# Kernel tuning notes

Measured on AMD Instinct MI355X. Metric: run time of the kernel, lower is better.

The kernel has to match this reference:

```python
import jax, jax.numpy as jnp
import numpy as np

N_NODES = 40000
N_EDGES = 1_600_000
F_DIM = 64          # num_features per node; MLP input is 2*F_DIM = 128
HIDDEN = 64
BETA = 1.0          # temperature tmp passed to concrete_sample


def setup_inputs() -> dict:
    key = jax.random.key(0)
    k_e, k_n, k_w1, k_w2 = jax.random.split(key, 4)
    # unique edge list (matches torch COO->dense semantics exactly: no duplicate coords)
    rng = np.random.default_rng(0)
    keys = np.unique(rng.integers(0, N_NODES * N_NODES, size=int(N_EDGES * 1.1), dtype=np.int64))
    assert keys.size >= N_EDGES
    keys = keys[:N_EDGES]
    col = jnp.asarray((keys // N_NODES).astype(np.int32))
    row = jnp.asarray((keys % N_NODES).astype(np.int32))
    embed = jax.random.normal(k_e, (N_NODES, F_DIM), jnp.float32)
    # torch.rand noise for the concrete/gumbel-sigmoid sample (kept strictly inside (0,1))
    noise = jax.random.uniform(k_n, (N_EDGES,), jnp.float32, 1e-6, 1.0 - 1e-6)
    lim1 = 1.0 / np.sqrt(2 * F_DIM)
    W1 = jax.random.uniform(k_w1, (2 * F_DIM, HIDDEN), jnp.float32, -lim1, lim1)
    b1 = jnp.zeros((HIDDEN,), jnp.float32)
    lim2 = 1.0 / np.sqrt(HIDDEN)
    W2 = jax.random.uniform(k_w2, (HIDDEN, 1), jnp.float32, -lim2, lim2)
    b2 = jnp.zeros((1,), jnp.float32)
    return {"embed": embed, "W1": W1, "b1": b1, "W2": W2, "b2": b2,
            "noise": noise, "col": col, "row": row}


def reference(embed, W1, b1, W2, b2, noise, col, row):
    # --- gather + concat + 2-layer MLP (elayers) ---
    f12 = jnp.concatenate([embed[col], embed[row]], axis=-1)   # [E, 2F]
    h = jax.nn.relu(f12 @ W1 + b1)                              # [E, 64]
    log_alpha = (h @ W2 + b2).reshape(-1)                       # [E]
    # --- concrete_sample, training=True, sample_bias=0 ---
    gate = jnp.log(noise) - jnp.log1p(-noise)
    values = jax.nn.sigmoid((gate + log_alpha) / BETA)          # sparse_mask_values
    # --- symmetrization: sym = (M + M^T)/2 gathered back at (col,row) ---
    # Equivalent to torch's sparse->dense->transpose->gather, but done sparsely
    # via a reverse-edge lookup on sorted pair keys (edges are unique).
    n = embed.shape[0]
    keys = col * n + row                                        # int32-safe: n*n < 2^31
    order = jnp.argsort(keys)
    skeys = keys[order]
    svals = values[order]
    rkeys = row * n + col
    pos = jnp.clip(jnp.searchsorted(skeys, rkeys), 0, keys.shape[0] - 1)
    rev = jnp.where(skeys[pos] == rkeys, svals[pos], jnp.float32(0.0))
    edge_mask = (values + rev) * 0.5
    return edge_mask
```

## Files before the change

### kernel.cpp

```cpp
#include <hip/hip_runtime.h>
#include <hip/hip_bf16.h>


typedef __attribute__((ext_vector_type(2))) float f32x2;

#define EPAD 68

__global__ __launch_bounds__(256) void precompute_kernel(
        const float* __restrict__ embed,
        const float* __restrict__ W1,
        const float* __restrict__ b1,
        unsigned* __restrict__ Ptop,
        unsigned* __restrict__ Pbot,
        int n_nodes) {
    int t = threadIdx.x;

    __shared__ float W1s[128 * 64];
    __shared__ float E[64 * EPAD];
    int base = blockIdx.x * 64;

#pragma unroll
    for (int i = 0; i < 8; ++i) {
        int idx = i * 256 + t;
        ((float4*)W1s)[idx] = ((const float4*)W1)[idx];
    }
#pragma unroll
    for (int i = 0; i < 4; ++i) {
        int fi = i * 256 + t;
        int n = fi >> 4;
        int k4 = (fi & 15) * 4;
        float4 v;
        if (base + n < n_nodes)
            v = ((const float4*)(embed + (size_t)(base + n) * 64))[fi & 15];
        else
            v = make_float4(0.f, 0.f, 0.f, 0.f);
        *((float4*)(E + n * EPAD + k4)) = v;
    }
    __syncthreads();

    int tj = t & 15, tn = t >> 4;
    int j4 = tj * 4, n4 = tn * 4;
    float4 b1v = *(const float4*)(b1 + j4);
    float4 at[4], ab[4];
#pragma unroll
    for (int i = 0; i < 4; ++i) {
        at[i] = b1v;
        ab[i] = make_float4(0.f, 0.f, 0.f, 0.f);
    }

#pragma unroll 2
    for (int k4 = 0; k4 < 64; k4 += 4) {
        float4 e[4], wt[4], wb[4];
#pragma unroll
        for (int i = 0; i < 4; ++i) {
            e[i]  = *(const float4*)(E + (n4 + i) * EPAD + k4);
            wt[i] = *(const float4*)(W1s + (k4 + i) * 64 + j4);
            wb[i] = *(const float4*)(W1s + (64 + k4 + i) * 64 + j4);
        }
#pragma unroll
        for (int n = 0; n < 4; ++n) {
#pragma unroll
            for (int kk = 0; kk < 4; ++kk) {
                float ev = (kk == 0) ? e[n].x : (kk == 1) ? e[n].y
                         : (kk == 2) ? e[n].z : e[n].w;
                at[n].x += ev * wt[kk].x;  at[n].y += ev * wt[kk].y;
                at[n].z += ev * wt[kk].z;  at[n].w += ev * wt[kk].w;
                ab[n].x += ev * wb[kk].x;  ab[n].y += ev * wb[kk].y;
                ab[n].z += ev * wb[kk].z;  ab[n].w += ev * wb[kk].w;
            }
        }
    }

#pragma unroll
    for (int i = 0; i < 4; ++i) {
        int node = base + n4 + i;
        if (node >= n_nodes) break;
        int wt8 = __builtin_amdgcn_cvt_pk_fp8_f32(at[i].x, at[i].y, 0, false);
        wt8     = __builtin_amdgcn_cvt_pk_fp8_f32(at[i].z, at[i].w, wt8, true);
        Ptop[(size_t)node * 16 + tj] = (unsigned)wt8;
        int wb8 = __builtin_amdgcn_cvt_pk_fp8_f32(ab[i].x, ab[i].y, 0, false);
        wb8     = __builtin_amdgcn_cvt_pk_fp8_f32(ab[i].z, ab[i].w, wb8, true);
        Pbot[(size_t)node * 16 + tj] = (unsigned)wb8;
    }
}

#define DOTW(au, bu, wp, acc0, acc1) do {                             \
    f32x2 alo = __builtin_amdgcn_cvt_pk_f32_fp8((au), false);         \
    f32x2 ahi = __builtin_amdgcn_cvt_pk_f32_fp8((au), true);          \
    f32x2 blo = __builtin_amdgcn_cvt_pk_f32_fp8((bu), false);         \
    f32x2 bhi = __builtin_amdgcn_cvt_pk_f32_fp8((bu), true);          \
    f32x2 s0 = alo + blo, s1 = ahi + bhi;                             \
    s0 = __builtin_elementwise_max(s0, (f32x2)0.f);                   \
    s1 = __builtin_elementwise_max(s1, (f32x2)0.f);                   \
    acc0 += s0 * ((const f32x2*)(wp))[0];                             \
    acc1 += s1 * ((const f32x2*)(wp))[1];                             \
} while (0)

__global__ __launch_bounds__(256) void edge_value_kernel(
        const uint4* __restrict__ Ptop,
        const uint4* __restrict__ Pbot,
        const float* __restrict__ W2,
        const float* __restrict__ b2,
        const float* __restrict__ noise,
        const int* __restrict__ col,
        const int* __restrict__ row,
        unsigned short* __restrict__ row16,
        unsigned short* __restrict__ vals16,
        int* __restrict__ rowptr,
        int n_edges, int n_nodes, int rp_blocks) {
    int t = threadIdx.x;
    int bid = blockIdx.x;

    if (bid < rp_blocks) {
        int v = bid * 256 + t;
        if (v <= n_nodes) {
            int lo = 0, hi = n_edges;
            while (lo < hi) {
                int mid = (lo + hi) >> 1;
                if (col[mid] < v) lo = mid + 1; else hi = mid;
            }
            rowptr[v] = lo;
        }
        return;
    }

    int e = (bid - rp_blocks) * 256 + t;
    if (e >= n_edges) return;
    int c = col[e], r = row[e];
    const uint4* pt = Ptop + (size_t)c * 4;
    const uint4* pb = Pbot + (size_t)r * 4;
    f32x2 acc0 = {b2[0], 0.f}, acc1 = {0.f, 0.f};
    f32x2 acc2 = {0.f, 0.f},  acc3 = {0.f, 0.f};
#pragma unroll
    for (int g = 0; g < 4; ++g) {
        uint4 a = pt[g];
        uint4 b = pb[g];
        const float* w = W2 + g * 16;
        DOTW(a.x, b.x, w,      acc0, acc1);
        DOTW(a.y, b.y, w + 4,  acc2, acc3);
        DOTW(a.z, b.z, w + 8,  acc0, acc1);
        DOTW(a.w, b.w, w + 12, acc2, acc3);
    }
    f32x2 acc = (acc0 + acc1) + (acc2 + acc3);
    float la = acc.x + acc.y;
    float u = noise[e];
    float v = u / (u + (1.f - u) * __expf(-la));
    unsigned q = (unsigned)(v * 65535.f + 0.5f);
    if (q > 65535u) q = 65535u;
    row16[e]  = (unsigned short)r;
    vals16[e] = (unsigned short)q;
}

__device__ __forceinline__ float rev_scan(const unsigned short* __restrict__ row16,
                                          const unsigned short* __restrict__ vals16,
                                          int c, int lo, int hi, int g, int rv) {
    if (rv < c) {
        while (++g < hi) { rv = row16[g]; if (rv >= c) break; }
        return (g < hi && rv == c) ? (float)vals16[g] : 0.f;
    } else {
        while (rv > c && g > lo) rv = row16[--g];
        return (rv == c) ? (float)vals16[g] : 0.f;
    }
}

__global__ __launch_bounds__(256) void symmetrize_kernel(
        const int* __restrict__ col,
        const unsigned short* __restrict__ row16,
        const unsigned short* __restrict__ vals16,
        const int* __restrict__ rowptr,
        float* __restrict__ out,
        int n_edges, float inv_n) {
    int t = threadIdx.x;
    int e0 = blockIdx.x * 1024 + t;
    int c[4], r[4], lo[4], hi[4], g[4], pr[4];
    float vq[4];
    bool p[4], s[4];

#pragma unroll
    for (int i = 0; i < 4; ++i) {
        int e = e0 + i * 256;
        p[i] = e < n_edges;
        c[i] = 0; r[i] = 0; vq[i] = 0.f;
        if (p[i]) {
            c[i]  = col[e];
            r[i]  = row16[e];
            vq[i] = (float)vals16[e];
        }
    }
#pragma unroll
    for (int i = 0; i < 4; ++i) {
        lo[i] = 0; hi[i] = 0;
        if (p[i]) { lo[i] = rowptr[r[i]]; hi[i] = rowptr[r[i] + 1]; }
    }
#pragma unroll
    for (int i = 0; i < 4; ++i) {
        s[i] = p[i] && hi[i] > lo[i];
        g[i] = 0; pr[i] = 0;
        if (s[i]) {
            g[i] = lo[i] + (int)((float)c[i] * (float)(hi[i] - lo[i]) * inv_n);
            if (g[i] >= hi[i]) g[i] = hi[i] - 1;
            pr[i] = row16[g[i]];
        }
    }
#pragma unroll
    for (int i = 0; i < 4; ++i) {
        if (!p[i]) continue;
        float rev = s[i] ? rev_scan(row16, vals16, c[i], lo[i], hi[i], g[i], pr[i]) : 0.f;
        out[e0 + i * 256] = (vq[i] + rev) * (0.5f / 65535.f);
    }
}

extern "C" void kernel_launch(void* const* d_in, const int* in_sizes, int n_in,
                              void* d_out, int out_size, void* d_ws, size_t ws_size,
                              hipStream_t stream) {
    const float* embed = (const float*)d_in[0];
    const float* W1    = (const float*)d_in[1];
    const float* b1    = (const float*)d_in[2];
    const float* W2    = (const float*)d_in[3];
    const float* b2    = (const float*)d_in[4];
    const float* noise = (const float*)d_in[5];
    const int*   col   = (const int*)d_in[6];
    const int*   row   = (const int*)d_in[7];

    int n_nodes = in_sizes[0] / 64;
    int n_edges = in_sizes[5];
    float* out = (float*)d_out;

    char* ws = (char*)d_ws;
    size_t p_sz   = (size_t)n_nodes * 16 * sizeof(unsigned);
    size_t e16_sz = (size_t)n_edges * sizeof(unsigned short);
    unsigned*       Ptop   = (unsigned*)ws;
    unsigned*       Pbot   = (unsigned*)(ws + p_sz);
    unsigned short* row16  = (unsigned short*)(ws + 2 * p_sz);
    unsigned short* vals16 = (unsigned short*)(ws + 2 * p_sz + e16_sz);
    int*            rowptr = (int*)(ws + 2 * p_sz + 2 * e16_sz);

    int gemm_blocks = (n_nodes + 63) / 64;
    int rp_blocks   = (n_nodes + 256) / 256;

    precompute_kernel<<<gemm_blocks, 256, 0, stream>>>(
        embed, W1, b1, Ptop, Pbot, n_nodes);

    edge_value_kernel<<<rp_blocks + (n_edges + 255) / 256, 256, 0, stream>>>(
        (const uint4*)Ptop, (const uint4*)Pbot, W2, b2, noise, col, row,
        row16, vals16, rowptr, n_edges, n_nodes, rp_blocks);

    symmetrize_kernel<<<(n_edges + 1023) / 1024, 256, 0, stream>>>(
        col, row16, vals16, rowptr, out, n_edges, 1.0f / (float)n_nodes);
}
```

Measured before the change: 72.41 us.

## Write half-values in edge kernel and symmetrize only upper-triangle edges pairwise

The edge kernel now writes each edge's own half-value (or the full value on the diagonal) straight to the output. The symmetrize kernel handles only edges with col < row: it searches for the reverse edge and, on a match, adds each partner's contribution to both output slots. This roughly halves the reverse-edge searches and skips the output writes for unmatched edges. In exchange it uses read-modify-write updates to the output and scattered writes to the matched index, and its own value is now taken from the full-precision float rather than the 16-bit quantized copy.

```diff
diff --git a/kernel.cpp b/kernel.cpp
--- a/kernel.cpp
+++ b/kernel.cpp
@@ -106,6 +106,7 @@
         const int* __restrict__ row,
         unsigned short* __restrict__ row16,
         unsigned short* __restrict__ vals16,
+        float* __restrict__ out,
         int* __restrict__ rowptr,
         int n_edges, int n_nodes, int rp_blocks) {
     int t = threadIdx.x;
@@ -149,18 +150,7 @@
     if (q > 65535u) q = 65535u;
     row16[e]  = (unsigned short)r;
     vals16[e] = (unsigned short)q;
-}
-
-__device__ __forceinline__ float rev_scan(const unsigned short* __restrict__ row16,
-                                          const unsigned short* __restrict__ vals16,
-                                          int c, int lo, int hi, int g, int rv) {
-    if (rv < c) {
-        while (++g < hi) { rv = row16[g]; if (rv >= c) break; }
-        return (g < hi && rv == c) ? (float)vals16[g] : 0.f;
-    } else {
-        while (rv > c && g > lo) rv = row16[--g];
-        return (rv == c) ? (float)vals16[g] : 0.f;
-    }
+    out[e] = (c == r) ? v : 0.5f * v;
 }
 
 __global__ __launch_bounds__(256) void symmetrize_kernel(
@@ -173,28 +163,24 @@
     int t = threadIdx.x;
     int e0 = blockIdx.x * 1024 + t;
     int c[4], r[4], lo[4], hi[4], g[4], pr[4];
-    float vq[4];
-    bool p[4], s[4];
+    bool act[4], s[4];
 
 #pragma unroll
     for (int i = 0; i < 4; ++i) {
         int e = e0 + i * 256;
-        p[i] = e < n_edges;
-        c[i] = 0; r[i] = 0; vq[i] = 0.f;
-        if (p[i]) {
-            c[i]  = col[e];
-            r[i]  = row16[e];
-            vq[i] = (float)vals16[e];
-        }
+        bool p = e < n_edges;
+        c[i] = 0; r[i] = -1;
+        if (p) { c[i] = col[e]; r[i] = row16[e]; }
+        act[i] = p && c[i] < r[i];
     }
 #pragma unroll
     for (int i = 0; i < 4; ++i) {
         lo[i] = 0; hi[i] = 0;
-        if (p[i]) { lo[i] = rowptr[r[i]]; hi[i] = rowptr[r[i] + 1]; }
-    }
-#pragma unroll
-    for (int i = 0; i < 4; ++i) {
-        s[i] = p[i] && hi[i] > lo[i];
+        if (act[i]) { lo[i] = rowptr[r[i]]; hi[i] = rowptr[r[i] + 1]; }
+    }
+#pragma unroll
+    for (int i = 0; i < 4; ++i) {
+        s[i] = act[i] && hi[i] > lo[i];
         g[i] = 0; pr[i] = 0;
         if (s[i]) {
             g[i] = lo[i] + (int)((float)c[i] * (float)(hi[i] - lo[i]) * inv_n);
@@ -204,9 +190,23 @@
     }
 #pragma unroll
     for (int i = 0; i < 4; ++i) {
-        if (!p[i]) continue;
-        float rev = s[i] ? rev_scan(row16, vals16, c[i], lo[i], hi[i], g[i], pr[i]) : 0.f;
-        out[e0 + i * 256] = (vq[i] + rev) * (0.5f / 65535.f);
+        if (!s[i]) continue;
+        int gg = g[i], rv = pr[i], hh = hi[i], ll = lo[i], cc = c[i];
+        int match = -1;
+        if (rv < cc) {
+            while (++gg < hh) { rv = row16[gg]; if (rv >= cc) break; }
+            if (gg < hh && rv == cc) match = gg;
+        } else {
+            while (rv > cc && gg > ll) rv = row16[--gg];
+            if (rv == cc) match = gg;
+        }
+        if (match >= 0) {
+            int e = e0 + i * 256;
+            float theirs = (float)vals16[match] * (0.5f / 65535.f);
+            float mine   = (float)vals16[e]     * (0.5f / 65535.f);
+            out[e]     += theirs;
+            out[match] += mine;
+        }
     }
 }
 
@@ -243,7 +243,7 @@
 
     edge_value_kernel<<<rp_blocks + (n_edges + 255) / 256, 256, 0, stream>>>(
         (const uint4*)Ptop, (const uint4*)Pbot, W2, b2, noise, col, row,
-        row16, vals16, rowptr, n_edges, n_nodes, rp_blocks);
+        row16, vals16, out, rowptr, n_edges, n_nodes, rp_blocks);
 
     symmetrize_kernel<<<(n_edges + 1023) / 1024, 256, 0, stream>>>(
         col, row16, vals16, rowptr, out, n_edges, 1.0f / (float)n_nodes);
```

New measurement: 62.62 us. 1.16x faster.
